# Optimization experiments

Measured on AMD Instinct MI355X. Metric: run time of the kernel, lower is better.

The kernel has to match this reference:

```python
import jax, jax.numpy as jnp
import numpy as np

R = 10  # num_relations
NUM_GRAPHS = 64


def rgcn_layer(x, W, root, b, src, dst, etype):
    # x: [N, Din], W: [R, Din, H], root: [Din, H], b: [H]
    N = x.shape[0]
    H = W.shape[-1]
    # per-relation transform of all nodes: [R, N, H]
    h_all = jnp.einsum('nd,rdh->rnh', x, W)
    # gather transformed source features per edge by its relation: [E, H]
    msg = h_all[etype, src]
    # mean-aggregate per (dst, relation) pair, then sum over relations (PyG RGCNConv semantics)
    key = dst * R + etype
    sums = jax.ops.segment_sum(msg, key, num_segments=N * R)  # [N*R, H]
    cnt = jax.ops.segment_sum(jnp.ones((etype.shape[0],), x.dtype), key, num_segments=N * R)
    agg = (sums.reshape(N, R, H) / jnp.clip(cnt.reshape(N, R, 1), 1.0, None)).sum(axis=1)
    return agg + x @ root + b


def setup_inputs() -> dict:
    key = jax.random.key(0)
    ks = jax.random.split(key, 12)
    N, E, DIN, H = 100000, 3200000, 128, 64
    x = jax.random.normal(ks[0], (N, DIN), dtype=jnp.float32)
    edge_index = jax.random.randint(ks[1], (2, E), 0, N, dtype=jnp.int64)
    edge_type = jax.random.randint(ks[2], (E,), 0, R, dtype=jnp.int64)
    batch = jnp.sort(jax.random.randint(ks[3], (N,), 0, NUM_GRAPHS, dtype=jnp.int64))
    s1 = 1.0 / np.sqrt(DIN)
    s2 = 1.0 / np.sqrt(H)
    W1 = jax.random.uniform(ks[4], (R, DIN, H), jnp.float32, -s1, s1)
    root1 = jax.random.uniform(ks[5], (DIN, H), jnp.float32, -s1, s1)
    b1 = jnp.zeros((H,), jnp.float32)
    W2 = jax.random.uniform(ks[6], (R, H, H), jnp.float32, -s2, s2)
    root2 = jax.random.uniform(ks[7], (H, H), jnp.float32, -s2, s2)
    b2 = jnp.zeros((H,), jnp.float32)
    cls_w = jax.random.uniform(ks[8], (H, 1), jnp.float32, -s2, s2)
    cls_b = jnp.zeros((1,), jnp.float32)
    return {"x": x, "edge_index": edge_index, "edge_type": edge_type, "batch": batch,
            "W1": W1, "root1": root1, "b1": b1, "W2": W2, "root2": root2, "b2": b2,
            "cls_w": cls_w, "cls_b": cls_b}


def reference(x, edge_index, edge_type, batch, W1, root1, b1, W2, root2, b2, cls_w, cls_b):
    src, dst = edge_index[0], edge_index[1]
    h = jax.nn.relu(rgcn_layer(x, W1, root1, b1, src, dst, edge_type))   # dropout = identity (eval)
    h = jax.nn.relu(rgcn_layer(h, W2, root2, b2, src, dst, edge_type))
    # global mean pool per graph
    sums = jax.ops.segment_sum(h, batch, num_segments=NUM_GRAPHS)        # [G, H]
    cnt = jax.ops.segment_sum(jnp.ones((h.shape[0],), h.dtype), batch, num_segments=NUM_GRAPHS)
    pooled = sums / jnp.clip(cnt[:, None], 1.0, None)
    out = pooled @ cls_w + cls_b                                          # [G, 1]
    return out.reshape(-1)
```

## Files before the change

### kernel.cpp

```cpp
#include <hip/hip_runtime.h>

#define R_REL 10
#define HD 64
#define BSH 8
#define KPB (256 * R_REL)
#define SORT_CAP 12288

typedef __attribute__((ext_vector_type(8))) short short8;
typedef __attribute__((ext_vector_type(4))) float floatx4;
typedef __attribute__((ext_vector_type(8))) unsigned short ushort8;

__device__ inline unsigned short f32_to_bf16_rne(float f) {
    unsigned int u = __float_as_uint(f);
    unsigned int r = (u + 0x7FFFu + ((u >> 16) & 1u)) >> 16;
    return (unsigned short)r;
}
__device__ inline float bf16_to_f32(unsigned short h) {
    return __uint_as_float(((unsigned int)h) << 16);
}
__device__ inline float bf16lo(unsigned int u) { return __uint_as_float(u << 16); }
__device__ inline float bf16hi(unsigned int u) { return __uint_as_float(u & 0xFFFF0000u); }

__device__ __forceinline__ void gload_lds16(const unsigned short* g, unsigned short* l) {
    __builtin_amdgcn_global_load_lds(
        (const __attribute__((address_space(1))) unsigned int*)g,
        (__attribute__((address_space(3))) unsigned int*)l, 16, 0, 0);
}

__global__ __launch_bounds__(256) void bhist_kernel(const int* __restrict__ dst,
                                                    int* __restrict__ bcnt, int E) {
    __shared__ int l[512];
    int t = threadIdx.x;
    l[t] = 0; l[t + 256] = 0;
    __syncthreads();
    int e0 = blockIdx.x * 4096;
    for (int i = t; i < 4096; i += 256) {
        int e = e0 + i;
        if (e < E) atomicAdd(&l[dst[e] >> BSH], 1);
    }
    __syncthreads();
    if (l[t]) atomicAdd(&bcnt[t], l[t]);
    if (l[t + 256]) atomicAdd(&bcnt[t + 256], l[t + 256]);
}

__global__ void bscan_kernel(const int* __restrict__ bcnt, int* __restrict__ boff,
                             int* __restrict__ gcursor, int NBK, int E) {
    int t = threadIdx.x;
    int v = (t < NBK) ? bcnt[t] : 0;
    __shared__ int tmp[512];
    tmp[t] = v;
    __syncthreads();
    for (int off = 1; off < 512; off <<= 1) {
        int u = (t >= off) ? tmp[t - off] : 0;
        __syncthreads();
        tmp[t] += u;
        __syncthreads();
    }
    int excl = tmp[t] - v;
    if (t < NBK) { boff[t] = excl; gcursor[t] = excl; }
    if (t == 0) boff[NBK] = E;
}

__global__ __launch_bounds__(256) void bscatter_kernel(const int* __restrict__ src,
                                                       const int* __restrict__ dst,
                                                       const int* __restrict__ et,
                                                       int* __restrict__ gcursor,
                                                       int2* __restrict__ staged, int E) {
    __shared__ int lcnt[512];
    __shared__ int lbase[512];
    int t = threadIdx.x;
    int e0 = blockIdx.x * 4096;
    lcnt[t] = 0; lcnt[t + 256] = 0;
    __syncthreads();
    for (int i = t; i < 4096; i += 256) {
        int e = e0 + i;
        if (e < E) atomicAdd(&lcnt[dst[e] >> BSH], 1);
    }
    __syncthreads();
    int c0 = lcnt[t], c1 = lcnt[t + 256];
    lbase[t]       = (c0 > 0) ? atomicAdd(&gcursor[t], c0) : 0;
    lbase[t + 256] = (c1 > 0) ? atomicAdd(&gcursor[t + 256], c1) : 0;
    lcnt[t] = 0; lcnt[t + 256] = 0;
    __syncthreads();
    for (int i = t; i < 4096; i += 256) {
        int e = e0 + i;
        if (e < E) {
            int dd = dst[e];
            int bk = dd >> BSH;
            int pos = lbase[bk] + atomicAdd(&lcnt[bk], 1);
            staged[pos] = make_int2(src[e], dd * R_REL + et[e]);
        }
    }
}

__global__ __launch_bounds__(256) void sortfill_kernel(const int2* __restrict__ staged,
                                                       const int* __restrict__ boff,
                                                       int* __restrict__ dcnt,
                                                       int2* __restrict__ edata,
                                                       int N, int Ntot) {
    __shared__ int hist[KPB];
    __shared__ float wkey[KPB];
    __shared__ int part[256];
    __shared__ int lsrc[SORT_CAP];
    __shared__ unsigned short lkey[SORT_CAP];
    int t = threadIdx.x, b = blockIdx.x;
    int s0 = boff[b], s1 = boff[b + 1];
    int keylo = b * KPB;
#pragma unroll
    for (int j = 0; j < KPB / 256; ++j) hist[t + j * 256] = 0;
    __syncthreads();
    for (int i = s0 + t; i < s1; i += 256)
        atomicAdd(&hist[staged[i].y - keylo], 1);
    __syncthreads();
    int base = t * (KPB / 256);
    int c[KPB / 256];
    int s = 0;
#pragma unroll
    for (int j = 0; j < KPB / 256; ++j) {
        c[j] = hist[base + j]; s += c[j];
        wkey[base + j] = 1.0f / fmaxf((float)c[j], 1.0f);
    }
    int dglob = b * 256 + t;
    if (dglob < Ntot) dcnt[dglob] = s;
    part[t] = s;
    __syncthreads();
    for (int off = 1; off < 256; off <<= 1) {
        int u = (t >= off) ? part[t - off] : 0;
        __syncthreads();
        part[t] += u;
        __syncthreads();
    }
    int run = part[t] - s;
#pragma unroll
    for (int j = 0; j < KPB / 256; ++j) { hist[base + j] = run; run += c[j]; }
    __syncthreads();
    for (int i = s0 + t; i < s1; i += 256) {
        int2 p = staged[i];
        int lk = p.y - keylo;
        int pos = atomicAdd(&hist[lk], 1);
        if (pos < SORT_CAP) { lsrc[pos] = p.x; lkey[pos] = (unsigned short)lk; }
        else {
            int rel = lk % R_REL;
            edata[s0 + pos] = make_int2(rel * N + p.x, __float_as_int(wkey[lk]));
        }
    }
    __syncthreads();
    int m = min(s1 - s0, SORT_CAP);
    for (int j = t; j < m; j += 256) {
        int lk = lkey[j];
        int rel = lk % R_REL;
        edata[s0 + j] = make_int2(rel * N + lsrc[j], __float_as_int(wkey[lk]));
    }
}

__global__ void scan1_kernel(const int* __restrict__ cnt, int* __restrict__ bsum, int M) {
    int b = blockIdx.x, tid = threadIdx.x;
    int base = b * 1024 + tid * 4;
    int s = 0;
#pragma unroll
    for (int j = 0; j < 4; ++j) { int i = base + j; if (i < M) s += cnt[i]; }
    for (int off = 32; off > 0; off >>= 1) s += __shfl_down(s, off);
    __shared__ int wsum[4];
    int lane = tid & 63, wid = tid >> 6;
    if (lane == 0) wsum[wid] = s;
    __syncthreads();
    if (tid == 0) bsum[b] = wsum[0] + wsum[1] + wsum[2] + wsum[3];
}

__global__ void scan2_kernel(const int* __restrict__ bsum, int* __restrict__ boff, int NB) {
    int tid = threadIdx.x;
    int lane = tid & 63, wid = tid >> 6;
    int v = (tid < NB) ? bsum[tid] : 0;
    int x = v;
    for (int off = 1; off < 64; off <<= 1) { int u = __shfl_up(x, off); if (lane >= off) x += u; }
    __shared__ int wsum[16];
    if (lane == 63) wsum[wid] = x;
    __syncthreads();
    int woff = 0;
    for (int w = 0; w < wid; ++w) woff += wsum[w];
    if (tid < NB) boff[tid] = x + woff - v;
}

__global__ void scan3_kernel(const int* __restrict__ cnt, const int* __restrict__ boff,
                             int* __restrict__ rowptr, int M) {
    int b = blockIdx.x, tid = threadIdx.x;
    int base = b * 1024 + tid * 4;
    int c[4]; int s = 0;
#pragma unroll
    for (int j = 0; j < 4; ++j) { int i = base + j; c[j] = (i < M) ? cnt[i] : 0; s += c[j]; }
    int lane = tid & 63, wid = tid >> 6;
    int x = s;
    for (int off = 1; off < 64; off <<= 1) { int u = __shfl_up(x, off); if (lane >= off) x += u; }
    __shared__ int wsum[4];
    if (lane == 63) wsum[wid] = x;
    __syncthreads();
    int woff = 0;
    for (int w = 0; w < wid; ++w) woff += wsum[w];
    int run = boff[b] + x + woff - s;
#pragma unroll
    for (int j = 0; j < 4; ++j) {
        int i = base + j;
        if (i < M) {
            rowptr[i] = run; run += c[j];
            if (i == M - 1) rowptr[M] = run;
        }
    }
}

__global__ void split_kernel(const float* __restrict__ src, unsigned short* __restrict__ hi,
                             unsigned short* __restrict__ lo, int n) {
    int i = blockIdx.x * 256 + threadIdx.x;
    if (i < n) {
        float v = src[i];
        unsigned short h = f32_to_bf16_rne(v);
        hi[i] = h;
        lo[i] = f32_to_bf16_rne(v - bf16_to_f32(h));
    }
}

__global__ void wsplit_kernel(const float* __restrict__ W, const float* __restrict__ root,
                              unsigned short* __restrict__ hi, unsigned short* __restrict__ lo,
                              int K) {
    int idx = blockIdx.x * 256 + threadIdx.x;
    int total = (R_REL + 1) * HD * K;
    if (idx >= total) return;
    int rel = idx / (HD * K);
    int rem = idx - rel * HD * K;
    int n = rem / K, k = rem - n * K;
    float v = (rel < R_REL) ? W[((size_t)rel * K + k) * HD + n] : root[(size_t)k * HD + n];
    unsigned short h = f32_to_bf16_rne(v);
    int ks = k ^ ((n & 7) << 3);
    int widx = rel * HD * K + n * K + ks;
    hi[widx] = h;
    lo[widx] = f32_to_bf16_rne(v - bf16_to_f32(h));
}

template <int K>
__global__ __launch_bounds__(512, 4)
void gemm_mfma(const unsigned short* __restrict__ Xhi,
               const unsigned short* __restrict__ Xlo,
               const unsigned short* __restrict__ Wthi,
               const unsigned short* __restrict__ Wtlo,
               unsigned short* __restrict__ hout,
               float* __restrict__ fout, int N) {
    constexpr int NS = K / 32;
    constexpr int TILE_SH = HD * K;
    constexpr int TILEB = TILE_SH * 2;
    constexpr int HALFC = K / 8;
    __shared__ unsigned short wlds[4 * TILE_SH];
    const int tid = threadIdx.x;
    const int w = tid >> 6, lane = tid & 63;
    const int quad = lane >> 4, l16 = lane & 15;
    const int n0 = blockIdx.x * 128;
    const int node = n0 + w * 16 + l16;
    const bool valid = node < N;

    short8 Xh[NS], Xl[NS];
#pragma unroll
    for (int s = 0; s < NS; ++s) {
        short8 z;
#pragma unroll
        for (int q = 0; q < 8; ++q) z[q] = 0;
        Xh[s] = z; Xl[s] = z;
        if (valid) {
            Xh[s] = *(const short8*)(Xhi + (size_t)node * K + s * 32 + quad * 8);
            Xl[s] = *(const short8*)(Xlo + (size_t)node * K + s * 32 + quad * 8);
        }
    }

    auto stage = [&](int rel, int b) {
        const unsigned short* hsrc = Wthi + (size_t)rel * TILE_SH;
        const unsigned short* lsrc = Wtlo + (size_t)rel * TILE_SH;
        unsigned short* dst0 = wlds + b * 2 * TILE_SH;
#pragma unroll
        for (int j = 0; j < NS; ++j) {
            int q = j * 8 + w;
            const unsigned short* src = (q < HALFC) ? (hsrc + q * 512)
                                                    : (lsrc + (q - HALFC) * 512);
            gload_lds16(src + lane * 8, dst0 + q * 512);
        }
    };

    stage(0, 0);
    __syncthreads();

    const int swzb = (l16 & 7) << 4;
    const size_t NHD = (size_t)N * HD;

#pragma unroll
    for (int c = 0; c <= R_REL; ++c) {
        const int cur = c & 1;
        if (c < R_REL) stage(c + 1, cur ^ 1);
        const char* wb = (const char*)(wlds + cur * 2 * TILE_SH);
        floatx4 acc[4];
#pragma unroll
        for (int mt = 0; mt < 4; ++mt) { floatx4 z = {0.f, 0.f, 0.f, 0.f}; acc[mt] = z; }
#pragma unroll
        for (int s = 0; s < NS; ++s) {
            const int koffb = ((s * 32 + quad * 8) * 2) ^ swzb;
#pragma unroll
            for (int mt = 0; mt < 4; ++mt) {
                const int rowb = (mt * 16 + l16) * (K * 2);
                short8 Wh = *(const short8*)(wb + rowb + koffb);
                short8 Wl = *(const short8*)(wb + TILEB + rowb + koffb);
                acc[mt] = __builtin_amdgcn_mfma_f32_16x16x32_bf16(Wh, Xh[s], acc[mt], 0, 0, 0);
                acc[mt] = __builtin_amdgcn_mfma_f32_16x16x32_bf16(Wh, Xl[s], acc[mt], 0, 0, 0);
                acc[mt] = __builtin_amdgcn_mfma_f32_16x16x32_bf16(Wl, Xh[s], acc[mt], 0, 0, 0);
            }
        }
        if (valid) {
            if (c < R_REL) {
                unsigned short* hp = hout + (size_t)c * NHD + (size_t)node * HD + quad * 4;
#pragma unroll
                for (int mt = 0; mt < 4; ++mt) {
                    unsigned int d0 = (unsigned int)f32_to_bf16_rne(acc[mt][0]) |
                                      ((unsigned int)f32_to_bf16_rne(acc[mt][1]) << 16);
                    unsigned int d1 = (unsigned int)f32_to_bf16_rne(acc[mt][2]) |
                                      ((unsigned int)f32_to_bf16_rne(acc[mt][3]) << 16);
                    *(uint2*)(hp + mt * 16) = make_uint2(d0, d1);
                }
            } else {
                float* fp = fout + (size_t)node * HD + quad * 4;
#pragma unroll
                for (int mt = 0; mt < 4; ++mt)
                    *(floatx4*)(fp + mt * 16) = acc[mt];
            }
        }
        __syncthreads();
    }
}

__global__ __launch_bounds__(256) void agg_kernel(const unsigned short* __restrict__ hc,
                                                  const int* __restrict__ rowptr,
                                                  const int2* __restrict__ edata,
                                                  float* __restrict__ acc, int N) {
    int gid = blockIdx.x * 256 + threadIdx.x;
    int d = gid >> 6;
    if (d >= N) return;
    int lane = threadIdx.x & 63;
    int quarter = lane >> 4, l16 = lane & 15;
    int e0 = rowptr[d], e1 = rowptr[d + 1];
    int ne = e1 - e0;
    if (ne == 0) return;
    float s0 = 0.f, s1 = 0.f, s2 = 0.f, s3 = 0.f;
    for (int rb = 0; rb < ne; rb += 64) {
        int nthis = min(64, ne - rb);
        int2 ed = make_int2(0, 0);
        if (lane < nthis) ed = edata[e0 + rb + lane];
        int off = ed.x << 6;
        float wv = __int_as_float(ed.y);
        for (int j = 0; j < nthis; j += 8) {
            int   oa = __shfl(off, j + quarter);
            float wa = __shfl(wv,  j + quarter);
            int   ob = __shfl(off, j + 4 + quarter);
            float wb = __shfl(wv,  j + 4 + quarter);
            uint2 da = *(const uint2*)(hc + oa + l16 * 4);
            uint2 db = *(const uint2*)(hc + ob + l16 * 4);
            s0 += wa * bf16lo(da.x); s1 += wa * bf16hi(da.x);
            s2 += wa * bf16lo(da.y); s3 += wa * bf16hi(da.y);
            s0 += wb * bf16lo(db.x); s1 += wb * bf16hi(db.x);
            s2 += wb * bf16lo(db.y); s3 += wb * bf16hi(db.y);
        }
    }
    s0 += __shfl_xor(s0, 16); s1 += __shfl_xor(s1, 16);
    s2 += __shfl_xor(s2, 16); s3 += __shfl_xor(s3, 16);
    s0 += __shfl_xor(s0, 32); s1 += __shfl_xor(s1, 32);
    s2 += __shfl_xor(s2, 32); s3 += __shfl_xor(s3, 32);
    if (lane < 16) {
        float4* ap = (float4*)(acc + (size_t)d * HD + l16 * 4);
        float4 a = *ap;
        a.x += s0; a.y += s1; a.z += s2; a.w += s3;
        *ap = a;
    }
}

__global__ void fin1_kernel(const float* __restrict__ acc, const float* __restrict__ bias,
                            unsigned short* __restrict__ hi, unsigned short* __restrict__ lo,
                            int NH) {
    int i = blockIdx.x * 256 + threadIdx.x;
    if (i < NH) {
        float v = fmaxf(acc[i] + bias[i & (HD - 1)], 0.f);
        unsigned short h = f32_to_bf16_rne(v);
        hi[i] = h;
        lo[i] = f32_to_bf16_rne(v - bf16_to_f32(h));
    }
}

__global__ __launch_bounds__(256) void pool_kernel(const float* __restrict__ acc,
                                                   const float* __restrict__ bias,
                                                   const int* __restrict__ batch,
                                                   float* __restrict__ pooled,
                                                   float* __restrict__ gcnt, int N) {
    int w = blockIdx.x * 4 + (threadIdx.x >> 6);
    int lane = threadIdx.x & 63;
    int base = w * 64;
    if (base >= N) return;
    int nn = min(64, N - base);
    float b = bias[lane];
    int g_l = (base + lane < N) ? batch[base + lane] : -1;
    int g_first = __shfl(g_l, 0);
    int g_last = __shfl(g_l, nn - 1);
    if (nn == 64 && g_first == g_last) {
        float p0 = 0.f, p1 = 0.f, p2 = 0.f, p3 = 0.f;
#pragma unroll
        for (int i = 0; i < 64; i += 4) {
            p0 += fmaxf(acc[(size_t)(base + i + 0) * HD + lane] + b, 0.f);
            p1 += fmaxf(acc[(size_t)(base + i + 1) * HD + lane] + b, 0.f);
            p2 += fmaxf(acc[(size_t)(base + i + 2) * HD + lane] + b, 0.f);
            p3 += fmaxf(acc[(size_t)(base + i + 3) * HD + lane] + b, 0.f);
        }
        atomicAdd(&pooled[g_first * HD + lane], (p0 + p1) + (p2 + p3));
        if (lane == 0) atomicAdd(&gcnt[g_first], 64.f);
    } else {
        int cur = g_first; float s = 0.f; int cnt = 0;
        for (int i = 0; i < nn; ++i) {
            int g = __shfl(g_l, i);
            if (g != cur) {
                atomicAdd(&pooled[cur * HD + lane], s);
                if (lane == 0) atomicAdd(&gcnt[cur], (float)cnt);
                cur = g; s = 0.f; cnt = 0;
            }
            s += fmaxf(acc[(size_t)(base + i) * HD + lane] + b, 0.f);
            cnt++;
        }
        atomicAdd(&pooled[cur * HD + lane], s);
        if (lane == 0) atomicAdd(&gcnt[cur], (float)cnt);
    }
}

__global__ void cls_kernel(const float* __restrict__ pooled, const float* __restrict__ gcnt,
                           const float* __restrict__ cls_w, const float* __restrict__ cls_b,
                           float* __restrict__ out) {
    int g = threadIdx.x;
    float invc = 1.0f / fmaxf(gcnt[g], 1.0f);
    float acc = 0.f;
    for (int j = 0; j < 64; ++j) acc += pooled[g * 64 + j] * cls_w[j];
    out[g] = acc * invc + cls_b[0];
}

extern "C" void kernel_launch(void* const* d_in, const int* in_sizes, int n_in,
                              void* d_out, int out_size, void* d_ws, size_t ws_size,
                              hipStream_t stream) {
    const float* x     = (const float*)d_in[0];
    const int*   eidx  = (const int*)d_in[1];
    const int*   et    = (const int*)d_in[2];
    const int*   batch = (const int*)d_in[3];
    const float* W1    = (const float*)d_in[4];
    const float* root1 = (const float*)d_in[5];
    const float* b1    = (const float*)d_in[6];
    const float* W2    = (const float*)d_in[7];
    const float* root2 = (const float*)d_in[8];
    const float* b2    = (const float*)d_in[9];
    const float* cls_w = (const float*)d_in[10];
    const float* cls_b = (const float*)d_in[11];

    const int N = in_sizes[3];
    const int E = in_sizes[2];
    const int NB = (N + 1023) / 1024;
    const int NBK = (N + (1 << BSH) - 1) >> BSH;
    const int* srcp = eidx;
    const int* dstp = eidx + E;

    char* ws = (char*)d_ws;
    size_t off = 0;
    auto alloc = [&](size_t bytes) -> void* {
        void* p = ws + off;
        off = (off + bytes + 255) & ~(size_t)255;
        return p;
    };
    unsigned short* Xhi  = (unsigned short*)alloc((size_t)N * 128 * 2);
    unsigned short* Xlo  = (unsigned short*)alloc((size_t)N * 128 * 2);
    float*          accb = (float*)alloc((size_t)N * HD * 4);
    unsigned short* Wt1hi = (unsigned short*)alloc((size_t)(R_REL + 1) * HD * 128 * 2);
    unsigned short* Wt1lo = (unsigned short*)alloc((size_t)(R_REL + 1) * HD * 128 * 2);
    unsigned short* Wt2hi = (unsigned short*)alloc((size_t)(R_REL + 1) * HD * HD * 2);
    unsigned short* Wt2lo = (unsigned short*)alloc((size_t)(R_REL + 1) * HD * HD * 2);
    int2*  edata  = (int2*)alloc((size_t)E * 8);
    int*   rowptr = (int*)alloc((size_t)(N + 1) * 4);
    int*   dcnt   = (int*)alloc((size_t)N * 4);
    int*   bsum   = (int*)alloc((size_t)NB * 4);
    int*   bofs   = (int*)alloc((size_t)NB * 4);
    int*   bcnt   = (int*)alloc(512 * 4);
    int*   bboff  = (int*)alloc(513 * 4);
    int*   gcur   = (int*)alloc(512 * 4);
    float* pooled = (float*)alloc((size_t)(64 * HD + 64) * 4);
    float* gcnt   = pooled + 64 * HD;
    unsigned short* h_chunk = (unsigned short*)alloc((size_t)R_REL * N * HD * 2);

    int2* staged = (int2*)Xhi;
    unsigned short* H1hi = Xhi;
    unsigned short* H1lo = Xlo;

    hipMemsetAsync(bcnt, 0, 512 * 4, stream);
    hipMemsetAsync(pooled, 0, (size_t)(64 * HD + 64) * 4, stream);

    int nchunks = (E + 4095) / 4096;
    bhist_kernel<<<nchunks, 256, 0, stream>>>(dstp, bcnt, E);
    bscan_kernel<<<1, 512, 0, stream>>>(bcnt, bboff, gcur, NBK, E);
    bscatter_kernel<<<nchunks, 256, 0, stream>>>(srcp, dstp, et, gcur, staged, E);
    sortfill_kernel<<<NBK, 256, 0, stream>>>(staged, bboff, dcnt, edata, N, N);
    scan1_kernel<<<NB, 256, 0, stream>>>(dcnt, bsum, N);
    scan2_kernel<<<1, 1024, 0, stream>>>(bsum, bofs, NB);
    scan3_kernel<<<NB, 256, 0, stream>>>(dcnt, bofs, rowptr, N);

    int NK = N * 128;
    split_kernel<<<(NK + 255) / 256, 256, 0, stream>>>(x, Xhi, Xlo, NK);
    int tw1 = (R_REL + 1) * HD * 128, tw2 = (R_REL + 1) * HD * HD;
    wsplit_kernel<<<(tw1 + 255) / 256, 256, 0, stream>>>(W1, root1, Wt1hi, Wt1lo, 128);
    wsplit_kernel<<<(tw2 + 255) / 256, 256, 0, stream>>>(W2, root2, Wt2hi, Wt2lo, HD);

    const int gemmBlocks = (N + 127) / 128;
    const int aggBlocks  = (int)(((size_t)N * 64 + 255) / 256);
    const int NH = N * HD;

    gemm_mfma<128><<<gemmBlocks, 512, 0, stream>>>(Xhi, Xlo, Wt1hi, Wt1lo, h_chunk, accb, N);
    agg_kernel<<<aggBlocks, 256, 0, stream>>>(h_chunk, rowptr, edata, accb, N);
    fin1_kernel<<<(NH + 255) / 256, 256, 0, stream>>>(accb, b1, H1hi, H1lo, NH);

    gemm_mfma<64><<<gemmBlocks, 512, 0, stream>>>(H1hi, H1lo, Wt2hi, Wt2lo, h_chunk, accb, N);
    agg_kernel<<<aggBlocks, 256, 0, stream>>>(h_chunk, rowptr, edata, accb, N);

    int poolWaves = (N + 63) / 64;
    pool_kernel<<<(poolWaves + 3) / 4, 256, 0, stream>>>(accb, b2, batch, pooled, gcnt, N);
    cls_kernel<<<1, 64, 0, stream>>>(pooled, gcnt, cls_w, cls_b, (float*)d_out);
}
```

Measured before the change: 631.3 us.

## Pack staged edges into 32-bit words, locally sort scatter, retile GEMM waves 2x2

The bucket scatter now packs the local key (dst-in-bucket*R+etype) and src into one 32-bit word instead of an int2. It also stages each 4096-edge chunk in LDS sorted by bucket, so the global writes become contiguous runs per bucket. This halves the staged traffic and improves write coalescing, at the cost of extra LDS and another scan. Separately, the MFMA GEMM splits its 8 waves into a 2x4 grid, with each wave covering 32 nodes by 32 outputs instead of 16 nodes by 64. Each LDS weight fragment is therefore reused across two node groups, which cuts LDS reads per MFMA while holding twice as many X registers.

```diff
diff --git a/kernel.cpp b/kernel.cpp
--- a/kernel.cpp
+++ b/kernel.cpp
@@ -65,35 +65,54 @@
                                                        const int* __restrict__ dst,
                                                        const int* __restrict__ et,
                                                        int* __restrict__ gcursor,
-                                                       int2* __restrict__ staged, int E) {
+                                                       unsigned int* __restrict__ staged,
+                                                       int E) {
     __shared__ int lcnt[512];
+    __shared__ int lstart[512];
     __shared__ int lbase[512];
+    __shared__ int tmp[256];
+    __shared__ unsigned int lbuf[4096];
+    __shared__ unsigned short lbkt[4096];
     int t = threadIdx.x;
     int e0 = blockIdx.x * 4096;
+    int nthis = min(4096, E - e0);
     lcnt[t] = 0; lcnt[t + 256] = 0;
     __syncthreads();
-    for (int i = t; i < 4096; i += 256) {
-        int e = e0 + i;
-        if (e < E) atomicAdd(&lcnt[dst[e] >> BSH], 1);
-    }
-    __syncthreads();
-    int c0 = lcnt[t], c1 = lcnt[t + 256];
-    lbase[t]       = (c0 > 0) ? atomicAdd(&gcursor[t], c0) : 0;
-    lbase[t + 256] = (c1 > 0) ? atomicAdd(&gcursor[t + 256], c1) : 0;
+    for (int i = t; i < nthis; i += 256) atomicAdd(&lcnt[dst[e0 + i] >> BSH], 1);
+    __syncthreads();
+    int c0 = lcnt[2 * t], c1 = lcnt[2 * t + 1];
+    int ps = c0 + c1;
+    tmp[t] = ps;
+    __syncthreads();
+    for (int off = 1; off < 256; off <<= 1) {
+        int u = (t >= off) ? tmp[t - off] : 0;
+        __syncthreads();
+        tmp[t] += u;
+        __syncthreads();
+    }
+    int ex = tmp[t] - ps;
+    lstart[2 * t] = ex; lstart[2 * t + 1] = ex + c0;
+    lbase[2 * t]     = (c0 > 0) ? atomicAdd(&gcursor[2 * t], c0) : 0;
+    lbase[2 * t + 1] = (c1 > 0) ? atomicAdd(&gcursor[2 * t + 1], c1) : 0;
+    __syncthreads();
     lcnt[t] = 0; lcnt[t + 256] = 0;
     __syncthreads();
-    for (int i = t; i < 4096; i += 256) {
-        int e = e0 + i;
-        if (e < E) {
-            int dd = dst[e];
-            int bk = dd >> BSH;
-            int pos = lbase[bk] + atomicAdd(&lcnt[bk], 1);
-            staged[pos] = make_int2(src[e], dd * R_REL + et[e]);
-        }
-    }
-}
-
-__global__ __launch_bounds__(256) void sortfill_kernel(const int2* __restrict__ staged,
+    for (int i = t; i < nthis; i += 256) {
+        int dd = dst[e0 + i];
+        int bk = dd >> BSH;
+        int lk = (dd & ((1 << BSH) - 1)) * R_REL + et[e0 + i];
+        unsigned int p = ((unsigned int)lk << 17) | (unsigned int)src[e0 + i];
+        int pos = lstart[bk] + atomicAdd(&lcnt[bk], 1);
+        lbuf[pos] = p; lbkt[pos] = (unsigned short)bk;
+    }
+    __syncthreads();
+    for (int i = t; i < nthis; i += 256) {
+        int bk = lbkt[i];
+        staged[lbase[bk] + i - lstart[bk]] = lbuf[i];
+    }
+}
+
+__global__ __launch_bounds__(256) void sortfill_kernel(const unsigned int* __restrict__ staged,
                                                        const int* __restrict__ boff,
                                                        int* __restrict__ dcnt,
                                                        int2* __restrict__ edata,
@@ -105,12 +124,11 @@
     __shared__ unsigned short lkey[SORT_CAP];
     int t = threadIdx.x, b = blockIdx.x;
     int s0 = boff[b], s1 = boff[b + 1];
-    int keylo = b * KPB;
 #pragma unroll
     for (int j = 0; j < KPB / 256; ++j) hist[t + j * 256] = 0;
     __syncthreads();
     for (int i = s0 + t; i < s1; i += 256)
-        atomicAdd(&hist[staged[i].y - keylo], 1);
+        atomicAdd(&hist[staged[i] >> 17], 1);
     __syncthreads();
     int base = t * (KPB / 256);
     int c[KPB / 256];
@@ -135,13 +153,13 @@
     for (int j = 0; j < KPB / 256; ++j) { hist[base + j] = run; run += c[j]; }
     __syncthreads();
     for (int i = s0 + t; i < s1; i += 256) {
-        int2 p = staged[i];
-        int lk = p.y - keylo;
+        unsigned int p = staged[i];
+        int lk = p >> 17;
         int pos = atomicAdd(&hist[lk], 1);
-        if (pos < SORT_CAP) { lsrc[pos] = p.x; lkey[pos] = (unsigned short)lk; }
+        if (pos < SORT_CAP) { lsrc[pos] = (int)(p & 0x1FFFFu); lkey[pos] = (unsigned short)lk; }
         else {
             int rel = lk % R_REL;
-            edata[s0 + pos] = make_int2(rel * N + p.x, __float_as_int(wkey[lk]));
+            edata[s0 + pos] = make_int2(rel * N + (int)(p & 0x1FFFFu), __float_as_int(wkey[lk]));
         }
     }
     __syncthreads();
@@ -251,20 +269,26 @@
     const int tid = threadIdx.x;
     const int w = tid >> 6, lane = tid & 63;
     const int quad = lane >> 4, l16 = lane & 15;
+    const int wr = w >> 2, wc = w & 3;
     const int n0 = blockIdx.x * 128;
-    const int node = n0 + w * 16 + l16;
-    const bool valid = node < N;
-
-    short8 Xh[NS], Xl[NS];
+    const int nodeA = n0 + wc * 32 + l16;
+    const int nodeB = nodeA + 16;
+    const bool vA = nodeA < N, vB = nodeB < N;
+
+    short8 Xh[2][NS], Xl[2][NS];
 #pragma unroll
     for (int s = 0; s < NS; ++s) {
         short8 z;
 #pragma unroll
         for (int q = 0; q < 8; ++q) z[q] = 0;
-        Xh[s] = z; Xl[s] = z;
-        if (valid) {
-            Xh[s] = *(const short8*)(Xhi + (size_t)node * K + s * 32 + quad * 8);
-            Xl[s] = *(const short8*)(Xlo + (size_t)node * K + s * 32 + quad * 8);
+        Xh[0][s] = z; Xl[0][s] = z; Xh[1][s] = z; Xl[1][s] = z;
+        if (vA) {
+            Xh[0][s] = *(const short8*)(Xhi + (size_t)nodeA * K + s * 32 + quad * 8);
+            Xl[0][s] = *(const short8*)(Xlo + (size_t)nodeA * K + s * 32 + quad * 8);
+        }
+        if (vB) {
+            Xh[1][s] = *(const short8*)(Xhi + (size_t)nodeB * K + s * 32 + quad * 8);
+            Xl[1][s] = *(const short8*)(Xlo + (size_t)nodeB * K + s * 32 + quad * 8);
         }
     }
 
@@ -292,38 +316,54 @@
         const int cur = c & 1;
         if (c < R_REL) stage(c + 1, cur ^ 1);
         const char* wb = (const char*)(wlds + cur * 2 * TILE_SH);
-        floatx4 acc[4];
-#pragma unroll
-        for (int mt = 0; mt < 4; ++mt) { floatx4 z = {0.f, 0.f, 0.f, 0.f}; acc[mt] = z; }
+        floatx4 acc[2][2];
+#pragma unroll
+        for (int mt = 0; mt < 2; ++mt) {
+            floatx4 z = {0.f, 0.f, 0.f, 0.f};
+            acc[mt][0] = z; acc[mt][1] = z;
+        }
 #pragma unroll
         for (int s = 0; s < NS; ++s) {
             const int koffb = ((s * 32 + quad * 8) * 2) ^ swzb;
 #pragma unroll
-            for (int mt = 0; mt < 4; ++mt) {
-                const int rowb = (mt * 16 + l16) * (K * 2);
+            for (int mt = 0; mt < 2; ++mt) {
+                const int rowb = (wr * 32 + mt * 16 + l16) * (K * 2);
                 short8 Wh = *(const short8*)(wb + rowb + koffb);
                 short8 Wl = *(const short8*)(wb + TILEB + rowb + koffb);
-                acc[mt] = __builtin_amdgcn_mfma_f32_16x16x32_bf16(Wh, Xh[s], acc[mt], 0, 0, 0);
-                acc[mt] = __builtin_amdgcn_mfma_f32_16x16x32_bf16(Wh, Xl[s], acc[mt], 0, 0, 0);
-                acc[mt] = __builtin_amdgcn_mfma_f32_16x16x32_bf16(Wl, Xh[s], acc[mt], 0, 0, 0);
+#pragma unroll
+                for (int nh = 0; nh < 2; ++nh) {
+                    acc[mt][nh] = __builtin_amdgcn_mfma_f32_16x16x32_bf16(Wh, Xh[nh][s], acc[mt][nh], 0, 0, 0);
+                    acc[mt][nh] = __builtin_amdgcn_mfma_f32_16x16x32_bf16(Wh, Xl[nh][s], acc[mt][nh], 0, 0, 0);
+                    acc[mt][nh] = __builtin_amdgcn_mfma_f32_16x16x32_bf16(Wl, Xh[nh][s], acc[mt][nh], 0, 0, 0);
+                }
             }
         }
-        if (valid) {
-            if (c < R_REL) {
-                unsigned short* hp = hout + (size_t)c * NHD + (size_t)node * HD + quad * 4;
-#pragma unroll
-                for (int mt = 0; mt < 4; ++mt) {
-                    unsigned int d0 = (unsigned int)f32_to_bf16_rne(acc[mt][0]) |
-                                      ((unsigned int)f32_to_bf16_rne(acc[mt][1]) << 16);
-                    unsigned int d1 = (unsigned int)f32_to_bf16_rne(acc[mt][2]) |
-                                      ((unsigned int)f32_to_bf16_rne(acc[mt][3]) << 16);
-                    *(uint2*)(hp + mt * 16) = make_uint2(d0, d1);
+        if (c < R_REL) {
+#pragma unroll
+            for (int mt = 0; mt < 2; ++mt) {
+#pragma unroll
+                for (int nh = 0; nh < 2; ++nh) {
+                    int node = (nh == 0) ? nodeA : nodeB;
+                    if (nh == 0 ? vA : vB) {
+                        unsigned int d0 = (unsigned int)f32_to_bf16_rne(acc[mt][nh][0]) |
+                                          ((unsigned int)f32_to_bf16_rne(acc[mt][nh][1]) << 16);
+                        unsigned int d1 = (unsigned int)f32_to_bf16_rne(acc[mt][nh][2]) |
+                                          ((unsigned int)f32_to_bf16_rne(acc[mt][nh][3]) << 16);
+                        *(uint2*)(hout + (size_t)c * NHD + (size_t)node * HD +
+                                  wr * 32 + mt * 16 + quad * 4) = make_uint2(d0, d1);
+                    }
                 }
-            } else {
-                float* fp = fout + (size_t)node * HD + quad * 4;
-#pragma unroll
-                for (int mt = 0; mt < 4; ++mt)
-                    *(floatx4*)(fp + mt * 16) = acc[mt];
+            }
+        } else {
+#pragma unroll
+            for (int mt = 0; mt < 2; ++mt) {
+#pragma unroll
+                for (int nh = 0; nh < 2; ++nh) {
+                    int node = (nh == 0) ? nodeA : nodeB;
+                    if (nh == 0 ? vA : vB)
+                        *(floatx4*)(fout + (size_t)node * HD + wr * 32 + mt * 16 + quad * 4) =
+                            acc[mt][nh];
+                }
             }
         }
         __syncthreads();
@@ -487,7 +527,7 @@
     float* gcnt   = pooled + 64 * HD;
     unsigned short* h_chunk = (unsigned short*)alloc((size_t)R_REL * N * HD * 2);
 
-    int2* staged = (int2*)Xhi;
+    unsigned int* staged = (unsigned int*)Xhi;
     unsigned short* H1hi = Xhi;
     unsigned short* H1lo = Xlo;
 
```

New measurement: 599.4 us. 1.05x faster.
